# Optimization experiments

Measured on AMD Instinct MI355X. Metric: run time of the kernel, lower is better.

## Reference

```python
import jax, jax.numpy as jnp
import numpy as np

B, N, K, U = 64, 4096, 32, 16
NUM_STEPS = 8
NUM_CLASSES = 2


def setup_inputs() -> dict:
    key = jax.random.key(0)
    ks = jax.random.split(key, 17)
    s = 0.05
    g = lambda k, shape: jax.random.normal(k, shape, dtype=jnp.float32) * s
    return {
        "inputs": jax.random.normal(ks[0], (B, N, K + 2), dtype=jnp.float32),
        # UGRNN cell params
        "Wn": g(ks[1], (K, U)),
        "Wg": g(ks[2], (U, U)), "Ug": g(ks[3], (U, U)), "bg": jnp.zeros((U,), jnp.float32),
        "Wc": g(ks[4], (U, U)), "Uc": g(ks[5], (U, U)), "bc": jnp.zeros((U,), jnp.float32),
        "We": g(ks[6], (U, U)), "be": jnp.zeros((U,), jnp.float32),
        # MLP head (Dropout is identity at inference)
        "W1": g(ks[7], (N * U, 256)), "b1": jnp.zeros((256,), jnp.float32),
        "W2": g(ks[8], (256, 32)),    "b2": jnp.zeros((32,), jnp.float32),
        "W3": g(ks[9], (32, NUM_CLASSES)), "b3": jnp.zeros((NUM_CLASSES,), jnp.float32),
    }


def reference(inputs, Wn, Wg, Ug, bg, Wc, Uc, bc, We, be, W1, b1, W2, b2, W3, b3):
    # split channels: node scalar, K neighbour features, edge scalar
    h0 = inputs[..., 0]            # [B, N]
    neigh = inputs[..., 1:-1]      # [B, N, K]
    e0 = inputs[..., -1]           # [B, N]

    units = Wg.shape[0]
    h = jnp.broadcast_to(h0[..., None], h0.shape + (units,))  # tile -> [B, N, U]
    e = jnp.broadcast_to(e0[..., None], e0.shape + (units,))  # tile -> [B, N, U]

    # neighbour aggregation/projection is constant across steps -> hoist
    m = jnp.einsum("bnk,ku->bnu", neigh, Wn)  # [B, N, U]

    for _ in range(NUM_STEPS):  # small fixed unroll over num_steps
        x = m + e
        g = jax.nn.sigmoid(x @ Wg + h @ Ug + bg)  # update gate
        c = jnp.tanh(x @ Wc + h @ Uc + bc)        # candidate
        h = g * h + (1.0 - g) * c                 # UGRNN update
        e = jnp.tanh(x @ We + be)                 # edge state update

    out = h.reshape(h.shape[0], -1)               # Flatten -> [B, N*U]
    out = jax.nn.relu(out @ W1 + b1)
    out = jax.nn.relu(out @ W2 + b2)
    return jax.nn.softmax(out @ W3 + b3, axis=-1)  # [B, num_classes]
```

## Files before the change

### kernel.cpp

```cpp
#include <hip/hip_runtime.h>

typedef _Float16 half8_t __attribute__((ext_vector_type(8)));
typedef _Float16 half4_t __attribute__((ext_vector_type(4)));
typedef __fp16   fp16x2  __attribute__((ext_vector_type(2)));
typedef float    f32x4  __attribute__((ext_vector_type(4)));

#define MFMA32(a, b, c) __builtin_amdgcn_mfma_f32_16x16x32_f16((a), (b), (c), 0, 0, 0)
#define MFMA16(a, b, c) __builtin_amdgcn_mfma_f32_16x16x16f16((a), (b), (c), 0, 0, 0)

__device__ __forceinline__ void load_lds16(const void* g, void* l) {
    __builtin_amdgcn_global_load_lds(
        (const __attribute__((address_space(1))) unsigned int*)g,
        (__attribute__((address_space(3))) unsigned int*)l, 16, 0, 0);
}
__device__ __forceinline__ void load_lds4(const void* g, void* l) {
    __builtin_amdgcn_global_load_lds(
        (const __attribute__((address_space(1))) unsigned int*)g,
        (__attribute__((address_space(3))) unsigned int*)l, 4, 0, 0);
}

__device__ __forceinline__ half4_t pk4(f32x4 v) {
    fp16x2 lo = __builtin_amdgcn_cvt_pkrtz(v[0], v[1]);
    fp16x2 hi = __builtin_amdgcn_cvt_pkrtz(v[2], v[3]);
    half4_t r;
    r[0] = (_Float16)lo[0]; r[1] = (_Float16)lo[1];
    r[2] = (_Float16)hi[0]; r[3] = (_Float16)hi[1];
    return r;
}

__global__
__attribute__((amdgpu_flat_work_group_size(256, 256)))
void ugrnn_mfma(
    const float* __restrict__ inputs,
    const float* __restrict__ Wn, const float* __restrict__ Wg,
    const float* __restrict__ Ug, const float* __restrict__ bg,
    const float* __restrict__ Wc, const float* __restrict__ Uc,
    const float* __restrict__ bc, const float* __restrict__ We,
    const float* __restrict__ be, _Float16* __restrict__ h_t)
{
    __shared__ float raw[4][2][1088];

    const int wave = threadIdx.x >> 6;
    const int lane = threadIdx.x & 63;
    const int t16  = lane & 15;
    const int q    = lane >> 4;

    const int pidx0 = blockIdx.x * 4 + wave;
    const int pidx1 = pidx0 + 4096;

    const float NL2E = -1.44269504f;
    const float TL2E =  2.88539008f;

    half8_t An;
#pragma unroll
    for (int i = 0; i < 8; ++i)
        An[i] = (_Float16)Wn[(q * 8 + i) * 16 + t16];

    half4_t Awg, Aug, Awc, Auc, Awe;
#pragma unroll
    for (int i = 0; i < 4; ++i) {
        const int k = 4 * q + i;
        Awg[i] = (_Float16)(Wg[k * 16 + t16] * NL2E);
        Aug[i] = (_Float16)(Ug[k * 16 + t16] * NL2E);
        Awc[i] = (_Float16)(Wc[k * 16 + t16] * TL2E);
        Auc[i] = (_Float16)(Uc[k * 16 + t16] * TL2E);
        Awe[i] = (_Float16)(We[k * 16 + t16] * TL2E);
    }
    f32x4 bgC, bcC, beC;
#pragma unroll
    for (int r = 0; r < 4; ++r) {
        bgC[r] = bg[4 * q + r] * NL2E;
        bcC[r] = bc[4 * q + r] * TL2E;
        beC[r] = be[4 * q + r] * TL2E;
    }

    const float* g0 = inputs + (size_t)pidx0 * 1088;
    const float* g1 = inputs + (size_t)pidx1 * 1088;
    float* buf0 = &raw[wave][0][0];
    float* buf1 = &raw[wave][1][0];

    f32x4 m0[2], h0a[2], e0a[2], m1[2], h1a[2], e1a[2];
    const f32x4 zc = {0.f, 0.f, 0.f, 0.f};

    auto init_pair = [&](const float* rt, f32x4* m, f32x4* h, f32x4* e) {
#pragma unroll
        for (int u2 = 0; u2 < 2; ++u2) {
            const float* rp = rt + u2 * 544;
            half8_t Bx;
#pragma unroll
            for (int i = 0; i < 8; ++i)
                Bx[i] = (_Float16)rp[t16 * 34 + 1 + q * 8 + i];
            m[u2] = MFMA32(An, Bx, zc);
            const float hv = rp[t16 * 34 + 0];
            const float ev = rp[t16 * 34 + 33];
            h[u2] = (f32x4){hv, hv, hv, hv};
            e[u2] = (f32x4){ev, ev, ev, ev};
        }
    };

    auto run_pair = [&](int pidx, f32x4* m, f32x4* h, f32x4* e) {
#pragma unroll 1
        for (int step = 0; step < 8; ++step) {
            f32x4 gp[2], cp[2], ep[2];
#pragma unroll
            for (int u2 = 0; u2 < 2; ++u2) {
                const f32x4 x = m[u2] + e[u2];
                half4_t xB = pk4(x);
                half4_t hB = pk4(h[u2]);
                gp[u2] = MFMA16(Aug, hB, MFMA16(Awg, xB, bgC));
                cp[u2] = MFMA16(Auc, hB, MFMA16(Awc, xB, bcC));
                if (step < 7) ep[u2] = MFMA16(Awe, xB, beC);
            }
#pragma unroll
            for (int u2 = 0; u2 < 2; ++u2) {
#pragma unroll
                for (int r = 0; r < 4; ++r) {
                    const float Ae = 1.0f + __builtin_amdgcn_exp2f(gp[u2][r]);
                    const float Be = 1.0f + __builtin_amdgcn_exp2f(cp[u2][r]);
                    if (step < 7) {
                        const float Ce = 1.0f + __builtin_amdgcn_exp2f(ep[u2][r]);
                        const float BC = Be * Ce;
                        const float rr = __builtin_amdgcn_rcpf(Ae * BC);
                        const float gv = rr * BC;
                        const float rb = rr * (Ae * Ce);
                        const float rc = rr * (Ae * Be);
                        const float cv = 1.0f - 2.0f * rb;
                        h[u2][r] = cv + gv * (h[u2][r] - cv);
                        e[u2][r] = 1.0f - 2.0f * rc;
                    } else {
                        const float rr = __builtin_amdgcn_rcpf(Ae * Be);
                        const float gv = rr * Be;
                        const float cv = 1.0f - 2.0f * (rr * Ae);
                        h[u2][r] = cv + gv * (h[u2][r] - cv);
                    }
                }
            }
        }
        const int b  = pidx >> 7;
        const int n0 = (pidx & 127) << 5;
#pragma unroll
        for (int u2 = 0; u2 < 2; ++u2)
            *(half4_t*)(h_t + (size_t)b * 65536
                            + (size_t)(n0 + u2 * 16 + t16) * 16 + 4 * q) =
                pk4(h[u2]);
    };

#pragma unroll
    for (int k2 = 0; k2 < 4; ++k2)
        load_lds16(g0 + k2 * 256 + lane * 4, buf0 + k2 * 256);
    load_lds4(g0 + 1024 + lane, buf0 + 1024);
    asm volatile("s_waitcnt vmcnt(0)" ::: "memory");
    __builtin_amdgcn_sched_barrier(0);
    init_pair(buf0, m0, h0a, e0a);

#pragma unroll
    for (int k2 = 0; k2 < 4; ++k2)
        load_lds16(g1 + k2 * 256 + lane * 4, buf1 + k2 * 256);
    load_lds4(g1 + 1024 + lane, buf1 + 1024);

    run_pair(pidx0, m0, h0a, e0a);

    asm volatile("s_waitcnt vmcnt(0)" ::: "memory");
    __builtin_amdgcn_sched_barrier(0);
    init_pair(buf1, m1, h1a, e1a);
    run_pair(pidx1, m1, h1a, e1a);
}

__global__
__attribute__((amdgpu_flat_work_group_size(512, 512), amdgpu_waves_per_eu(1, 2)))
void fc1_mfma(const _Float16* __restrict__ h_t, const float* __restrict__ W1,
              _Float16* __restrict__ partials)
{
    __shared__ float w1s[2][64][258];
    const int tid  = threadIdx.x;
    const int wave = tid >> 6;
    const int lane = tid & 63;
    const int t16  = lane & 15;
    const int q    = lane >> 4;
    const int i0   = blockIdx.x * 256;

    f32x4 acc[4][2];
#pragma unroll
    for (int mt = 0; mt < 4; ++mt)
#pragma unroll
        for (int nt = 0; nt < 2; ++nt)
            acc[mt][nt] = (f32x4){0.f, 0.f, 0.f, 0.f};

#pragma unroll
    for (int r = 0; r < 8; ++r) {
        int row = wave * 8 + r;
        load_lds16(W1 + (size_t)(i0 + row) * 256 + lane * 4, &w1s[0][row][0]);
    }
    __syncthreads();

#pragma unroll 1
    for (int c = 0; c < 4; ++c) {
        const int buf = c & 1;
        const int cb  = i0 + c * 64;

        half8_t A[2][4];
#pragma unroll
        for (int ks = 0; ks < 2; ++ks)
#pragma unroll
            for (int mt = 0; mt < 4; ++mt)
                A[ks][mt] = *(const half8_t*)(h_t
                    + (size_t)(mt * 16 + t16) * 65536 + cb + ks * 32 + q * 8);

        if (c < 3) {
#pragma unroll
            for (int r = 0; r < 8; ++r) {
                int row = wave * 8 + r;
                load_lds16(W1 + (size_t)(cb + 64 + row) * 256 + lane * 4,
                           &w1s[buf ^ 1][row][0]);
            }
        }

#pragma unroll
        for (int ks = 0; ks < 2; ++ks) {
#pragma unroll
            for (int nt = 0; nt < 2; ++nt) {
                int j = (wave * 2 + nt) * 16 + t16;
                half8_t Bf;
#pragma unroll
                for (int i = 0; i < 8; ++i)
                    Bf[i] = (_Float16)w1s[buf][ks * 32 + q * 8 + i][j];
#pragma unroll
                for (int mt = 0; mt < 4; ++mt)
                    acc[mt][nt] = MFMA32(A[ks][mt], Bf, acc[mt][nt]);
            }
        }
        __syncthreads();
    }

    _Float16* pb = partials + (size_t)blockIdx.x * 16384;
#pragma unroll
    for (int mt = 0; mt < 4; ++mt)
#pragma unroll
        for (int nt = 0; nt < 2; ++nt)
#pragma unroll
            for (int r = 0; r < 4; ++r)
                pb[(mt * 16 + 4 * q + r) * 256 + (wave * 2 + nt) * 16 + t16] =
                    (_Float16)acc[mt][nt][r];
}

__global__ __launch_bounds__(1024) void mlp_tail(
    const _Float16* __restrict__ partials, const float* __restrict__ b1,
    const float* __restrict__ W2, const float* __restrict__ b2,
    const float* __restrict__ W3, const float* __restrict__ b3,
    float* __restrict__ out)
{
    __shared__ float x1p[16][256];
    __shared__ float x1s[256];
    __shared__ float x2q[32][33];
    __shared__ float x2s[32];
    __shared__ float lg[2];
    const int b = blockIdx.x, tid = threadIdx.x;
    const int kg = tid >> 6, l64 = tid & 63;
    const int j0 = l64 * 4;

    const _Float16* p = partials + (size_t)(kg * 16) * 16384 + (size_t)b * 256 + j0;
    float s0 = 0.f, s1 = 0.f, s2 = 0.f, s3 = 0.f;
#pragma unroll
    for (int k = 0; k < 16; ++k) {
        half4_t v = *(const half4_t*)(p + (size_t)k * 16384);
        s0 += (float)v[0]; s1 += (float)v[1]; s2 += (float)v[2]; s3 += (float)v[3];
    }
    x1p[kg][j0 + 0] = s0;
    x1p[kg][j0 + 1] = s1;
    x1p[kg][j0 + 2] = s2;
    x1p[kg][j0 + 3] = s3;
    __syncthreads();

    if (tid < 256) {
        float t = b1[tid];
#pragma unroll
        for (int g = 0; g < 16; ++g) t += x1p[g][tid];
        x1s[tid] = fmaxf(t, 0.f);
    }
    __syncthreads();

    const int j2 = tid & 31, g2 = tid >> 5;
    float s = 0.f;
#pragma unroll
    for (int k = g2 * 8; k < g2 * 8 + 8; ++k) s += x1s[k] * W2[k * 32 + j2];
    x2q[g2][j2] = s;
    __syncthreads();
    if (tid < 32) {
        float t = b2[tid];
#pragma unroll
        for (int g = 0; g < 32; ++g) t += x2q[g][tid];
        x2s[tid] = fmaxf(t, 0.f);
    }
    __syncthreads();
    if (tid < 2) {
        float t = b3[tid];
#pragma unroll
        for (int k = 0; k < 32; ++k) t += x2s[k] * W3[k * 2 + tid];
        lg[tid] = t;
    }
    __syncthreads();
    if (tid == 0) {
        float mx = fmaxf(lg[0], lg[1]);
        float e0 = __expf(lg[0] - mx), e1 = __expf(lg[1] - mx);
        float inv = 1.0f / (e0 + e1);
        out[b * 2 + 0] = e0 * inv;
        out[b * 2 + 1] = e1 * inv;
    }
}

extern "C" void kernel_launch(void* const* d_in, const int* in_sizes, int n_in,
                              void* d_out, int out_size, void* d_ws, size_t ws_size,
                              hipStream_t stream) {
    const float* inputs = (const float*)d_in[0];
    const float* Wn = (const float*)d_in[1];
    const float* Wg = (const float*)d_in[2];
    const float* Ug = (const float*)d_in[3];
    const float* bg = (const float*)d_in[4];
    const float* Wc = (const float*)d_in[5];
    const float* Uc = (const float*)d_in[6];
    const float* bc = (const float*)d_in[7];
    const float* We = (const float*)d_in[8];
    const float* be = (const float*)d_in[9];
    const float* W1 = (const float*)d_in[10];
    const float* b1 = (const float*)d_in[11];
    const float* W2 = (const float*)d_in[12];
    const float* b2 = (const float*)d_in[13];
    const float* W3 = (const float*)d_in[14];
    const float* b3 = (const float*)d_in[15];
    float* out = (float*)d_out;

    _Float16* h_t      = (_Float16*)d_ws;
    _Float16* partials = (_Float16*)((char*)d_ws + (size_t)64 * 65536 * 2);

    ugrnn_mfma<<<1024, 256, 0, stream>>>(inputs, Wn, Wg, Ug, bg, Wc, Uc, bc,
                                         We, be, h_t);
    fc1_mfma<<<256, 512, 0, stream>>>(h_t, W1, partials);
    mlp_tail<<<64, 1024, 0, stream>>>(partials, b1, W2, b2, W3, b3, out);
}
```

Baseline: 188.6 us.

## Split UGRNN to one pair per wave and halve fc1 K-chunk per block

```diff
diff --git a/kernel.cpp b/kernel.cpp
--- a/kernel.cpp
+++ b/kernel.cpp
@@ -38,15 +38,23 @@
     const float* __restrict__ bc, const float* __restrict__ We,
     const float* __restrict__ be, _Float16* __restrict__ h_t)
 {
-    __shared__ float raw[4][2][1088];
+    __shared__ float raw[4][1088];
 
     const int wave = threadIdx.x >> 6;
     const int lane = threadIdx.x & 63;
     const int t16  = lane & 15;
     const int q    = lane >> 4;
 
-    const int pidx0 = blockIdx.x * 4 + wave;
-    const int pidx1 = pidx0 + 4096;
+    const int pair = blockIdx.x * 4 + wave;
+    const int b    = pair >> 7;
+    const int n0   = (pair & 127) << 5;
+
+    const float* gsrc = inputs + (size_t)pair * 1088;
+    float* buf = raw[wave];
+#pragma unroll
+    for (int k2 = 0; k2 < 4; ++k2)
+        load_lds16(gsrc + k2 * 256 + lane * 4, buf + k2 * 256);
+    load_lds4(gsrc + 1024 + lane, buf + 1024);
 
     const float NL2E = -1.44269504f;
     const float TL2E =  2.88539008f;
@@ -74,116 +82,88 @@
         beC[r] = be[4 * q + r] * TL2E;
     }
 
-    const float* g0 = inputs + (size_t)pidx0 * 1088;
-    const float* g1 = inputs + (size_t)pidx1 * 1088;
-    float* buf0 = &raw[wave][0][0];
-    float* buf1 = &raw[wave][1][0];
-
-    f32x4 m0[2], h0a[2], e0a[2], m1[2], h1a[2], e1a[2];
+    asm volatile("s_waitcnt vmcnt(0)" ::: "memory");
+    __builtin_amdgcn_sched_barrier(0);
+
+    f32x4 m[2], h[2], e[2];
     const f32x4 zc = {0.f, 0.f, 0.f, 0.f};
-
-    auto init_pair = [&](const float* rt, f32x4* m, f32x4* h, f32x4* e) {
+#pragma unroll
+    for (int u2 = 0; u2 < 2; ++u2) {
+        const float* rp = buf + u2 * 544;
+        half8_t Bx;
+#pragma unroll
+        for (int i = 0; i < 8; ++i)
+            Bx[i] = (_Float16)rp[t16 * 34 + 1 + q * 8 + i];
+        m[u2] = MFMA32(An, Bx, zc);
+        const float hv = rp[t16 * 34 + 0];
+        const float ev = rp[t16 * 34 + 33];
+        h[u2] = (f32x4){hv, hv, hv, hv};
+        e[u2] = (f32x4){ev, ev, ev, ev};
+    }
+
+#pragma unroll 1
+    for (int step = 0; step < 8; ++step) {
+        f32x4 gp[2], cp[2], ep[2];
 #pragma unroll
         for (int u2 = 0; u2 < 2; ++u2) {
-            const float* rp = rt + u2 * 544;
-            half8_t Bx;
-#pragma unroll
-            for (int i = 0; i < 8; ++i)
-                Bx[i] = (_Float16)rp[t16 * 34 + 1 + q * 8 + i];
-            m[u2] = MFMA32(An, Bx, zc);
-            const float hv = rp[t16 * 34 + 0];
-            const float ev = rp[t16 * 34 + 33];
-            h[u2] = (f32x4){hv, hv, hv, hv};
-            e[u2] = (f32x4){ev, ev, ev, ev};
+            const f32x4 x = m[u2] + e[u2];
+            half4_t xB = pk4(x);
+            half4_t hB = pk4(h[u2]);
+            gp[u2] = MFMA16(Aug, hB, MFMA16(Awg, xB, bgC));
+            cp[u2] = MFMA16(Auc, hB, MFMA16(Awc, xB, bcC));
+            if (step < 7) ep[u2] = MFMA16(Awe, xB, beC);
         }
-    };
-
-    auto run_pair = [&](int pidx, f32x4* m, f32x4* h, f32x4* e) {
-#pragma unroll 1
-        for (int step = 0; step < 8; ++step) {
-            f32x4 gp[2], cp[2], ep[2];
-#pragma unroll
-            for (int u2 = 0; u2 < 2; ++u2) {
-                const f32x4 x = m[u2] + e[u2];
-                half4_t xB = pk4(x);
-                half4_t hB = pk4(h[u2]);
-                gp[u2] = MFMA16(Aug, hB, MFMA16(Awg, xB, bgC));
-                cp[u2] = MFMA16(Auc, hB, MFMA16(Awc, xB, bcC));
-                if (step < 7) ep[u2] = MFMA16(Awe, xB, beC);
-            }
-#pragma unroll
-            for (int u2 = 0; u2 < 2; ++u2) {
-#pragma unroll
-                for (int r = 0; r < 4; ++r) {
-                    const float Ae = 1.0f + __builtin_amdgcn_exp2f(gp[u2][r]);
-                    const float Be = 1.0f + __builtin_amdgcn_exp2f(cp[u2][r]);
-                    if (step < 7) {
-                        const float Ce = 1.0f + __builtin_amdgcn_exp2f(ep[u2][r]);
-                        const float BC = Be * Ce;
-                        const float rr = __builtin_amdgcn_rcpf(Ae * BC);
-                        const float gv = rr * BC;
-                        const float rb = rr * (Ae * Ce);
-                        const float rc = rr * (Ae * Be);
-                        const float cv = 1.0f - 2.0f * rb;
-                        h[u2][r] = cv + gv * (h[u2][r] - cv);
-                        e[u2][r] = 1.0f - 2.0f * rc;
-                    } else {
-                        const float rr = __builtin_amdgcn_rcpf(Ae * Be);
-                        const float gv = rr * Be;
-                        const float cv = 1.0f - 2.0f * (rr * Ae);
-                        h[u2][r] = cv + gv * (h[u2][r] - cv);
-                    }
+#pragma unroll
+        for (int u2 = 0; u2 < 2; ++u2) {
+#pragma unroll
+            for (int r = 0; r < 4; ++r) {
+                const float Ae = 1.0f + __builtin_amdgcn_exp2f(gp[u2][r]);
+                const float Be = 1.0f + __builtin_amdgcn_exp2f(cp[u2][r]);
+                if (step < 7) {
+                    const float Ce = 1.0f + __builtin_amdgcn_exp2f(ep[u2][r]);
+                    const float BC = Be * Ce;
+                    const float rr = __builtin_amdgcn_rcpf(Ae * BC);
+                    const float gv = rr * BC;
+                    const float rb = rr * (Ae * Ce);
+                    const float rc = rr * (Ae * Be);
+                    const float cv = 1.0f - 2.0f * rb;
+                    h[u2][r] = cv + gv * (h[u2][r] - cv);
+                    e[u2][r] = 1.0f - 2.0f * rc;
+                } else {
+                    const float rr = __builtin_amdgcn_rcpf(Ae * Be);
+                    const float gv = rr * Be;
+                    const float cv = 1.0f - 2.0f * (rr * Ae);
+                    h[u2][r] = cv + gv * (h[u2][r] - cv);
                 }
             }
         }
-        const int b  = pidx >> 7;
-        const int n0 = (pidx & 127) << 5;
-#pragma unroll
-        for (int u2 = 0; u2 < 2; ++u2)
-            *(half4_t*)(h_t + (size_t)b * 65536
-                            + (size_t)(n0 + u2 * 16 + t16) * 16 + 4 * q) =
-                pk4(h[u2]);
-    };
-
-#pragma unroll
-    for (int k2 = 0; k2 < 4; ++k2)
-        load_lds16(g0 + k2 * 256 + lane * 4, buf0 + k2 * 256);
-    load_lds4(g0 + 1024 + lane, buf0 + 1024);
-    asm volatile("s_waitcnt vmcnt(0)" ::: "memory");
-    __builtin_amdgcn_sched_barrier(0);
-    init_pair(buf0, m0, h0a, e0a);
-
-#pragma unroll
-    for (int k2 = 0; k2 < 4; ++k2)
-        load_lds16(g1 + k2 * 256 + lane * 4, buf1 + k2 * 256);
-    load_lds4(g1 + 1024 + lane, buf1 + 1024);
-
-    run_pair(pidx0, m0, h0a, e0a);
-
-    asm volatile("s_waitcnt vmcnt(0)" ::: "memory");
-    __builtin_amdgcn_sched_barrier(0);
-    init_pair(buf1, m1, h1a, e1a);
-    run_pair(pidx1, m1, h1a, e1a);
+    }
+
+#pragma unroll
+    for (int u2 = 0; u2 < 2; ++u2)
+        *(half4_t*)(h_t + (size_t)b * 65536
+                        + (size_t)(n0 + u2 * 16 + t16) * 16 + 4 * q) =
+            pk4(h[u2]);
 }
 
 __global__
-__attribute__((amdgpu_flat_work_group_size(512, 512), amdgpu_waves_per_eu(1, 2)))
+__attribute__((amdgpu_flat_work_group_size(256, 256)))
 void fc1_mfma(const _Float16* __restrict__ h_t, const float* __restrict__ W1,
               _Float16* __restrict__ partials)
 {
-    __shared__ float w1s[2][64][258];
+    __shared__ float w1s[2][32][258];
     const int tid  = threadIdx.x;
     const int wave = tid >> 6;
     const int lane = tid & 63;
     const int t16  = lane & 15;
     const int q    = lane >> 4;
-    const int i0   = blockIdx.x * 256;
-
-    f32x4 acc[4][2];
+    const int i0   = blockIdx.x * 128;
+
+    f32x4 acc[4][4];
 #pragma unroll
     for (int mt = 0; mt < 4; ++mt)
 #pragma unroll
-        for (int nt = 0; nt < 2; ++nt)
+        for (int nt = 0; nt < 4; ++nt)
             acc[mt][nt] = (f32x4){0.f, 0.f, 0.f, 0.f};
 
 #pragma unroll
@@ -196,38 +176,33 @@
 #pragma unroll 1
     for (int c = 0; c < 4; ++c) {
         const int buf = c & 1;
-        const int cb  = i0 + c * 64;
-
-        half8_t A[2][4];
-#pragma unroll
-        for (int ks = 0; ks < 2; ++ks)
-#pragma unroll
-            for (int mt = 0; mt < 4; ++mt)
-                A[ks][mt] = *(const half8_t*)(h_t
-                    + (size_t)(mt * 16 + t16) * 65536 + cb + ks * 32 + q * 8);
+        const int cb  = i0 + c * 32;
+
+        half8_t A[4];
+#pragma unroll
+        for (int mt = 0; mt < 4; ++mt)
+            A[mt] = *(const half8_t*)(h_t
+                + (size_t)(mt * 16 + t16) * 65536 + cb + q * 8);
 
         if (c < 3) {
 #pragma unroll
             for (int r = 0; r < 8; ++r) {
                 int row = wave * 8 + r;
-                load_lds16(W1 + (size_t)(cb + 64 + row) * 256 + lane * 4,
+                load_lds16(W1 + (size_t)(cb + 32 + row) * 256 + lane * 4,
                            &w1s[buf ^ 1][row][0]);
             }
         }
 
 #pragma unroll
-        for (int ks = 0; ks < 2; ++ks) {
-#pragma unroll
-            for (int nt = 0; nt < 2; ++nt) {
-                int j = (wave * 2 + nt) * 16 + t16;
-                half8_t Bf;
-#pragma unroll
-                for (int i = 0; i < 8; ++i)
-                    Bf[i] = (_Float16)w1s[buf][ks * 32 + q * 8 + i][j];
-#pragma unroll
-                for (int mt = 0; mt < 4; ++mt)
-                    acc[mt][nt] = MFMA32(A[ks][mt], Bf, acc[mt][nt]);
-            }
+        for (int nt = 0; nt < 4; ++nt) {
+            int j = (wave * 4 + nt) * 16 + t16;
+            half8_t Bf;
+#pragma unroll
+            for (int i = 0; i < 8; ++i)
+                Bf[i] = (_Float16)w1s[buf][q * 8 + i][j];
+#pragma unroll
+            for (int mt = 0; mt < 4; ++mt)
+                acc[mt][nt] = MFMA32(A[mt], Bf, acc[mt][nt]);
         }
         __syncthreads();
     }
@@ -236,10 +211,10 @@
 #pragma unroll
     for (int mt = 0; mt < 4; ++mt)
 #pragma unroll
-        for (int nt = 0; nt < 2; ++nt)
+        for (int nt = 0; nt < 4; ++nt)
 #pragma unroll
             for (int r = 0; r < 4; ++r)
-                pb[(mt * 16 + 4 * q + r) * 256 + (wave * 2 + nt) * 16 + t16] =
+                pb[(mt * 16 + 4 * q + r) * 256 + (wave * 4 + nt) * 16 + t16] =
                     (_Float16)acc[mt][nt][r];
 }
 
@@ -258,10 +233,10 @@
     const int kg = tid >> 6, l64 = tid & 63;
     const int j0 = l64 * 4;
 
-    const _Float16* p = partials + (size_t)(kg * 16) * 16384 + (size_t)b * 256 + j0;
+    const _Float16* p = partials + (size_t)(kg * 32) * 16384 + (size_t)b * 256 + j0;
     float s0 = 0.f, s1 = 0.f, s2 = 0.f, s3 = 0.f;
 #pragma unroll
-    for (int k = 0; k < 16; ++k) {
+    for (int k = 0; k < 32; ++k) {
         half4_t v = *(const half4_t*)(p + (size_t)k * 16384);
         s0 += (float)v[0]; s1 += (float)v[1]; s2 += (float)v[2]; s3 += (float)v[3];
     }
@@ -332,8 +307,8 @@
     _Float16* h_t      = (_Float16*)d_ws;
     _Float16* partials = (_Float16*)((char*)d_ws + (size_t)64 * 65536 * 2);
 
-    ugrnn_mfma<<<1024, 256, 0, stream>>>(inputs, Wn, Wg, Ug, bg, Wc, Uc, bc,
+    ugrnn_mfma<<<2048, 256, 0, stream>>>(inputs, Wn, Wg, Ug, bg, Wc, Uc, bc,
                                          We, be, h_t);
-    fc1_mfma<<<256, 512, 0, stream>>>(h_t, W1, partials);
+    fc1_mfma<<<512, 256, 0, stream>>>(h_t, W1, partials);
     mlp_tail<<<64, 1024, 0, stream>>>(partials, b1, W2, b2, W3, b3, out);
 }
```

Result: faster. 184.6 us (-2.1%).
